# Kernel optimization log

Hardware: AMD Instinct MI355X
Metric: run time of the kernel (lower is better)

Reference implementation:

```python
import jax, jax.numpy as jnp
import numpy as np

N_EMBD = 1024
HEAD_SIZE = 64
B, T = 16, 2048


def setup_inputs() -> dict:
    key = jax.random.key(0)
    ks = jax.random.split(key, 7)
    s = 1.0 / np.sqrt(N_EMBD)
    return {
        "x": jax.random.normal(ks[0], (B, T, N_EMBD), dtype=jnp.float32),
        "Wq": jax.random.uniform(ks[1], (N_EMBD, HEAD_SIZE), jnp.float32, -s, s),
        "bq": jax.random.uniform(ks[2], (HEAD_SIZE,), jnp.float32, -s, s),
        "Wk": jax.random.uniform(ks[3], (N_EMBD, HEAD_SIZE), jnp.float32, -s, s),
        "bk": jax.random.uniform(ks[4], (HEAD_SIZE,), jnp.float32, -s, s),
        "Wv": jax.random.uniform(ks[5], (N_EMBD, HEAD_SIZE), jnp.float32, -s, s),
        "bv": jax.random.uniform(ks[6], (HEAD_SIZE,), jnp.float32, -s, s),
    }


def reference(x, Wq, bq, Wk, bk, Wv, bv):
    # x: [B, T, C]
    q = x @ Wq + bq          # [B, T, H]
    k = x @ Wk + bk          # [B, T, H]
    v = x @ Wv + bv          # [B, T, H]
    scale = k.shape[-1] ** -0.5
    wei = jnp.einsum("bth,bsh->bts", q, k) * scale  # [B, T, T]
    Tn = x.shape[1]
    causal = jnp.tril(jnp.ones((Tn, Tn), dtype=bool))
    wei = jnp.where(causal, wei, -jnp.inf)
    wei = jax.nn.softmax(wei, axis=-1)
    # dropout is identity in eval mode
    return jnp.einsum("bts,bsh->bth", wei, v)  # [B, T, H]
```

## Files before the change

kernel.cpp:

```cpp
#include <hip/hip_runtime.h>
#include <math.h>

#define BB 16
#define TT 2048
#define CC 1024
#define HH 64
#define MTOT (BB*TT)

typedef _Float16 f16;
typedef _Float16 f16x8 __attribute__((ext_vector_type(8)));
typedef float f32x4 __attribute__((ext_vector_type(4)));

#define WT_OFF 0
#define Q_OFF  196608
#define K_OFF  (Q_OFF + (size_t)MTOT*HH)
#define VT_OFF (K_OFF + (size_t)MTOT*HH)

__device__ __forceinline__ void async16(const void* g, void* l) {
    __builtin_amdgcn_global_load_lds(
        (const __attribute__((address_space(1))) unsigned int*)g,
        (__attribute__((address_space(3))) unsigned int*)l, 16, 0, 0);
}

__device__ __forceinline__ f16x8 cvt8(float4 u, float4 v) {
    f16x8 r;
    r[0] = (f16)u.x; r[1] = (f16)u.y; r[2] = (f16)u.z; r[3] = (f16)u.w;
    r[4] = (f16)v.x; r[5] = (f16)v.y; r[6] = (f16)v.z; r[7] = (f16)v.w;
    return r;
}

__global__ __launch_bounds__(256) void prep_kernel(
    const float* __restrict__ Wq, const float* __restrict__ Wk,
    const float* __restrict__ Wv, f16* __restrict__ ws)
{
    int e = blockIdx.x * 256 + threadIdx.x;
    int ng = e >> 10, k = e & 1023;
    int which = ng >> 6, n = ng & 63;
    const float* W = (which == 0) ? Wq : (which == 1) ? Wk : Wv;
    ws[WT_OFF + e] = (f16)W[k * HH + n];
}

__global__ __launch_bounds__(256, 2) void qkv_kernel(
    const float* __restrict__ x,
    const float* __restrict__ bq, const float* __restrict__ bk,
    const float* __restrict__ bv, f16* __restrict__ ws)
{
    __shared__ __align__(16) float Xs[64 * 64];
    __shared__ __align__(16) f16   Ws[192 * 64];
    __shared__ __align__(16) f16   Vt[64][72];

    const f16* wt = ws + WT_OFF;
    const int tid  = threadIdx.x;
    const int lane = tid & 63, w = tid >> 6;
    const int c = lane & 15, g = lane >> 4;
    const int m0 = blockIdx.x * 64;

    f32x4 acc[4][3];
    #pragma unroll
    for (int mt = 0; mt < 4; ++mt)
        #pragma unroll
        for (int j = 0; j < 3; ++j) acc[mt][j] = (f32x4){0.f, 0.f, 0.f, 0.f};

    for (int k0 = 0; k0 < CC; k0 += 64) {
        __syncthreads();
        #pragma unroll
        for (int i = 0; i < 4; ++i) {
            int G0 = (w * 4 + i) * 64;
            int G = G0 + lane;
            int r = G >> 4, q = G & 15;
            async16(x + (size_t)(m0 + r) * CC + k0 + ((q ^ (r & 15)) << 2),
                    Xs + G0 * 4);
        }
        #pragma unroll
        for (int i = 0; i < 6; ++i) {
            int G0 = (w * 6 + i) * 64;
            int G = G0 + lane;
            int r = G >> 3, q = G & 7;
            async16(wt + (size_t)r * CC + k0 + ((q ^ (r & 7)) << 3),
                    Ws + G0 * 8);
        }
        __syncthreads();

        #pragma unroll
        for (int kk = 0; kk < 2; ++kk) {
            f16x8 bfr[3];
            #pragma unroll
            for (int j = 0; j < 3; ++j) {
                int r = (3 * w + j) * 16 + c;
                int p = (kk * 4 + g) ^ (c & 7);
                bfr[j] = *(const f16x8*)(Ws + r * 64 + p * 8);
            }
            #pragma unroll
            for (int mt = 0; mt < 4; ++mt) {
                int r = mt * 16 + c;
                int q = kk * 8 + 2 * g;
                float4 f0 = *(const float4*)(Xs + r * 64 + (q ^ c) * 4);
                float4 f1 = *(const float4*)(Xs + r * 64 + ((q + 1) ^ c) * 4);
                f16x8 a = cvt8(f0, f1);
                #pragma unroll
                for (int j = 0; j < 3; ++j)
                    acc[mt][j] = __builtin_amdgcn_mfma_f32_16x16x32_f16(
                        a, bfr[j], acc[mt][j], 0, 0, 0);
            }
        }
    }

    #pragma unroll
    for (int j = 0; j < 3; ++j) {
        int nt = 3 * w + j;
        int plane = nt >> 2;
        int h = (nt & 3) * 16 + c;
        if (plane == 0) {
            float bias = bq[h];
            #pragma unroll
            for (int mt = 0; mt < 4; ++mt)
                #pragma unroll
                for (int r = 0; r < 4; ++r) {
                    int m = m0 + mt * 16 + 4 * g + r;
                    ws[Q_OFF + (size_t)m * HH + h] =
                        (f16)((acc[mt][j][r] + bias) * 0.125f);
                }
        } else if (plane == 1) {
            float bias = bk[h];
            #pragma unroll
            for (int mt = 0; mt < 4; ++mt)
                #pragma unroll
                for (int r = 0; r < 4; ++r) {
                    int m = m0 + mt * 16 + 4 * g + r;
                    ws[K_OFF + (size_t)m * HH + h] = (f16)(acc[mt][j][r] + bias);
                }
        } else {
            float bias = bv[h];
            #pragma unroll
            for (int mt = 0; mt < 4; ++mt)
                #pragma unroll
                for (int r = 0; r < 4; ++r)
                    Vt[h][mt * 16 + 4 * g + r] = (f16)(acc[mt][j][r] + bias);
        }
    }
    __syncthreads();
    {
        int h = tid >> 2, seg = tid & 3;
        f16* dst = ws + VT_OFF + (size_t)h * MTOT + m0 + seg * 16;
        *(f16x8*)dst       = *(f16x8*)&Vt[h][seg * 16];
        *(f16x8*)(dst + 8) = *(f16x8*)&Vt[h][seg * 16 + 8];
    }
}

__global__ __launch_bounds__(256, 2) void attn_kernel(
    const f16* __restrict__ ws, float* __restrict__ out)
{
    const f16* qp = ws + Q_OFF;
    const f16* kp = ws + K_OFF;
    const f16* vt = ws + VT_OFF;

    __shared__ __align__(16) f16 Qs[64 * 64];
    __shared__ __align__(16) f16 Ks[64 * 64];
    __shared__ __align__(16) f16 Vs[64 * 64];
    __shared__ __align__(16) f16 Ps[4][16][72];

    const int tid  = threadIdx.x;
    const int lane = tid & 63, w = tid >> 6;
    const int c = lane & 15, g = lane >> 4;

    const int id = blockIdx.x;
    const int r8 = id & 7, j = id >> 3;
    const int half = j >> 5, qr = j & 31;
    const int b  = 2 * r8 + half;
    const int qi = half ? (31 - qr) : qr;
    const int q0 = qi * 64;
    const size_t rowbase = (size_t)b * TT;

    #pragma unroll
    for (int i = 0; i < 2; ++i) {
        int G0 = (w * 2 + i) * 64;
        int G = G0 + lane;
        int r = G >> 3, q = G & 7;
        async16(qp + (rowbase + q0 + r) * HH + ((q ^ (r & 7)) << 3),
                Qs + G0 * 8);
    }

    f32x4 o[5];
    #pragma unroll
    for (int nt = 0; nt < 5; ++nt) o[nt] = (f32x4){0.f, 0.f, 0.f, 0.f};

    f16x8 onesf;
    #pragma unroll
    for (int i = 0; i < 8; ++i) onesf[i] = (c == 0) ? (f16)1.0f : (f16)0.0f;

    for (int st = 0; st <= qi; ++st) {
        const int s0 = st * 64;
        __syncthreads();
        #pragma unroll
        for (int i = 0; i < 2; ++i) {
            int G0 = (w * 2 + i) * 64;
            int G = G0 + lane;
            int r = G >> 3, q = G & 7;
            int sw = (q ^ (r & 7)) << 3;
            async16(kp + (rowbase + s0 + r) * HH + sw, Ks + G0 * 8);
            async16(vt + (size_t)r * MTOT + rowbase + s0 + sw, Vs + G0 * 8);
        }
        __syncthreads();

        f16x8 aq[2];
        {
            int r = w * 16 + c;
            aq[0] = *(const f16x8*)(Qs + r * 64 + ((g)     ^ (c & 7)) * 8);
            aq[1] = *(const f16x8*)(Qs + r * 64 + ((4 + g) ^ (c & 7)) * 8);
        }

        f32x4 s[4];
        #pragma unroll
        for (int nt = 0; nt < 4; ++nt) {
            s[nt] = (f32x4){0.f, 0.f, 0.f, 0.f};
            int r = nt * 16 + c;
            f16x8 b0 = *(const f16x8*)(Ks + r * 64 + ((g)     ^ (c & 7)) * 8);
            f16x8 b1 = *(const f16x8*)(Ks + r * 64 + ((4 + g) ^ (c & 7)) * 8);
            s[nt] = __builtin_amdgcn_mfma_f32_16x16x32_f16(aq[0], b0, s[nt], 0, 0, 0);
            s[nt] = __builtin_amdgcn_mfma_f32_16x16x32_f16(aq[1], b1, s[nt], 0, 0, 0);
        }

        if (st == qi) {
            #pragma unroll
            for (int nt = 0; nt < 4; ++nt)
                #pragma unroll
                for (int rr = 0; rr < 4; ++rr)
                    if (nt * 16 + c > w * 16 + 4 * g + rr) s[nt][rr] = -INFINITY;
        }

        #pragma unroll
        for (int nt = 0; nt < 4; ++nt)
            #pragma unroll
            for (int rr = 0; rr < 4; ++rr)
                Ps[w][4 * g + rr][nt * 16 + c] = (f16)__expf(s[nt][rr]);
        f16x8 pa0 = *(f16x8*)&Ps[w][c][g * 8];
        f16x8 pa1 = *(f16x8*)&Ps[w][c][32 + g * 8];

        #pragma unroll
        for (int nt = 0; nt < 4; ++nt) {
            int r = nt * 16 + c;
            f16x8 v0 = *(const f16x8*)(Vs + r * 64 + ((g)     ^ (c & 7)) * 8);
            f16x8 v1 = *(const f16x8*)(Vs + r * 64 + ((4 + g) ^ (c & 7)) * 8);
            o[nt] = __builtin_amdgcn_mfma_f32_16x16x32_f16(pa0, v0, o[nt], 0, 0, 0);
            o[nt] = __builtin_amdgcn_mfma_f32_16x16x32_f16(pa1, v1, o[nt], 0, 0, 0);
        }
        o[4] = __builtin_amdgcn_mfma_f32_16x16x32_f16(pa0, onesf, o[4], 0, 0, 0);
        o[4] = __builtin_amdgcn_mfma_f32_16x16x32_f16(pa1, onesf, o[4], 0, 0, 0);
    }

    #pragma unroll
    for (int rr = 0; rr < 4; ++rr) {
        float lv = __shfl(o[4][rr], lane & 48);
        float inv = 1.0f / lv;
        int mrow = q0 + w * 16 + 4 * g + rr;
        #pragma unroll
        for (int nt = 0; nt < 4; ++nt)
            out[(rowbase + mrow) * HH + nt * 16 + c] = o[nt][rr] * inv;
    }
}

extern "C" void kernel_launch(void* const* d_in, const int* in_sizes, int n_in,
                              void* d_out, int out_size, void* d_ws, size_t ws_size,
                              hipStream_t stream) {
    const float* x  = (const float*)d_in[0];
    const float* Wq = (const float*)d_in[1];
    const float* bq = (const float*)d_in[2];
    const float* Wk = (const float*)d_in[3];
    const float* bk = (const float*)d_in[4];
    const float* Wv = (const float*)d_in[5];
    const float* bv = (const float*)d_in[6];
    f16*   ws  = (f16*)d_ws;
    float* out = (float*)d_out;

    prep_kernel<<<768, 256, 0, stream>>>(Wq, Wk, Wv, ws);
    qkv_kernel<<<MTOT / 64, 256, 0, stream>>>(x, bq, bk, bv, ws);
    dim3 g2(512);
    attn_kernel<<<g2, 256, 0, stream>>>(ws, out);
}
```

Measured before the change: 242.9 us.

## Double-buffer K/V and X/W tiles with manual waitcnt; transpose weights via LDS

```diff
diff --git a/kernel.cpp b/kernel.cpp
--- a/kernel.cpp
+++ b/kernel.cpp
@@ -8,6 +8,7 @@
 #define MTOT (BB*TT)
 
 typedef _Float16 f16;
+typedef _Float16 f16x4 __attribute__((ext_vector_type(4)));
 typedef _Float16 f16x8 __attribute__((ext_vector_type(8)));
 typedef float f32x4 __attribute__((ext_vector_type(4)));
 
@@ -16,28 +17,48 @@
 #define K_OFF  (Q_OFF + (size_t)MTOT*HH)
 #define VT_OFF (K_OFF + (size_t)MTOT*HH)
 
+#define WAITV(n) asm volatile("s_waitcnt vmcnt(" #n ")" ::: "memory")
+#define WAITLGKM0 asm volatile("s_waitcnt lgkmcnt(0)" ::: "memory")
+
+__device__ __forceinline__ void bar_raw() {
+    asm volatile("" ::: "memory");
+    __builtin_amdgcn_s_barrier();
+    asm volatile("" ::: "memory");
+}
+
 __device__ __forceinline__ void async16(const void* g, void* l) {
     __builtin_amdgcn_global_load_lds(
         (const __attribute__((address_space(1))) unsigned int*)g,
         (__attribute__((address_space(3))) unsigned int*)l, 16, 0, 0);
 }
 
-__device__ __forceinline__ f16x8 cvt8(float4 u, float4 v) {
-    f16x8 r;
-    r[0] = (f16)u.x; r[1] = (f16)u.y; r[2] = (f16)u.z; r[3] = (f16)u.w;
-    r[4] = (f16)v.x; r[5] = (f16)v.y; r[6] = (f16)v.z; r[7] = (f16)v.w;
-    return r;
-}
-
 __global__ __launch_bounds__(256) void prep_kernel(
     const float* __restrict__ Wq, const float* __restrict__ Wk,
     const float* __restrict__ Wv, f16* __restrict__ ws)
 {
-    int e = blockIdx.x * 256 + threadIdx.x;
-    int ng = e >> 10, k = e & 1023;
-    int which = ng >> 6, n = ng & 63;
+    __shared__ f16 Ls[64][72];
+    const int which = blockIdx.x >> 4, k0 = (blockIdx.x & 15) * 64;
     const float* W = (which == 0) ? Wq : (which == 1) ? Wk : Wv;
-    ws[WT_OFF + e] = (f16)W[k * HH + n];
+    const int t = threadIdx.x;
+    const int kr = t >> 2, cb = t & 3;
+    #pragma unroll
+    for (int i = 0; i < 4; ++i) {
+        float4 v = *(const float4*)(W + (size_t)(k0 + kr) * HH + cb * 16 + i * 4);
+        Ls[kr][cb * 16 + i * 4 + 0] = (f16)v.x;
+        Ls[kr][cb * 16 + i * 4 + 1] = (f16)v.y;
+        Ls[kr][cb * 16 + i * 4 + 2] = (f16)v.z;
+        Ls[kr][cb * 16 + i * 4 + 3] = (f16)v.w;
+    }
+    __syncthreads();
+    const int n = t >> 2, kc = (t & 3) * 16;
+    f16x8 o0, o1;
+    #pragma unroll
+    for (int i = 0; i < 8; ++i) o0[i] = Ls[kc + i][n];
+    #pragma unroll
+    for (int i = 0; i < 8; ++i) o1[i] = Ls[kc + 8 + i][n];
+    f16* dst = ws + WT_OFF + (size_t)(which * 64 + n) * CC + k0 + kc;
+    *(f16x8*)dst = o0;
+    *(f16x8*)(dst + 8) = o1;
 }
 
 __global__ __launch_bounds__(256, 2) void qkv_kernel(
@@ -45,9 +66,9 @@
     const float* __restrict__ bq, const float* __restrict__ bk,
     const float* __restrict__ bv, f16* __restrict__ ws)
 {
-    __shared__ __align__(16) float Xs[64 * 64];
-    __shared__ __align__(16) f16   Ws[192 * 64];
-    __shared__ __align__(16) f16   Vt[64][72];
+    __shared__ __align__(16) f16 XsL[2][64 * 64];
+    __shared__ __align__(16) f16 WsL[2][192 * 64];
+    __shared__ __align__(16) f16 Vt[64][72];
 
     const f16* wt = ws + WT_OFF;
     const int tid  = threadIdx.x;
@@ -61,47 +82,70 @@
         #pragma unroll
         for (int j = 0; j < 3; ++j) acc[mt][j] = (f32x4){0.f, 0.f, 0.f, 0.f};
 
-    for (int k0 = 0; k0 < CC; k0 += 64) {
-        __syncthreads();
-        #pragma unroll
-        for (int i = 0; i < 4; ++i) {
-            int G0 = (w * 4 + i) * 64;
-            int G = G0 + lane;
-            int r = G >> 4, q = G & 15;
-            async16(x + (size_t)(m0 + r) * CC + k0 + ((q ^ (r & 15)) << 2),
-                    Xs + G0 * 4);
-        }
-        #pragma unroll
-        for (int i = 0; i < 6; ++i) {
-            int G0 = (w * 6 + i) * 64;
-            int G = G0 + lane;
-            int r = G >> 3, q = G & 7;
-            async16(wt + (size_t)r * CC + k0 + ((q ^ (r & 7)) << 3),
-                    Ws + G0 * 8);
-        }
-        __syncthreads();
-
+    float4 xr[4];
+
+    #pragma unroll
+    for (int i = 0; i < 4; ++i)
+        xr[i] = *(const float4*)(x + (size_t)(m0 + w * 16 + 4 * i + g) * CC + 4 * c);
+    #pragma unroll
+    for (int i = 0; i < 6; ++i) {
+        int G = (w * 6 + i) * 64 + lane;
+        int r = G >> 3, q = G & 7;
+        async16(wt + (size_t)r * CC + ((q ^ (r & 7)) << 3), &WsL[0][(w * 6 + i) * 512]);
+    }
+    #pragma unroll
+    for (int i = 0; i < 4; ++i) {
+        int r = w * 16 + 4 * i + g;
+        f16x4 h; h[0] = (f16)xr[i].x; h[1] = (f16)xr[i].y;
+                 h[2] = (f16)xr[i].z; h[3] = (f16)xr[i].w;
+        *(f16x4*)((char*)&XsL[0][0] + r * 128 + (((c >> 1) ^ (r & 7)) << 4) + (c & 1) * 8) = h;
+    }
+    __syncthreads();
+
+    for (int t = 0; t < 16; ++t) {
+        const int p = t & 1;
+        if (t < 15) {
+            const int k0 = (t + 1) * 64;
+            #pragma unroll
+            for (int i = 0; i < 4; ++i)
+                xr[i] = *(const float4*)(x + (size_t)(m0 + w * 16 + 4 * i + g) * CC + k0 + 4 * c);
+            #pragma unroll
+            for (int i = 0; i < 6; ++i) {
+                int G = (w * 6 + i) * 64 + lane;
+                int r = G >> 3, q = G & 7;
+                async16(wt + (size_t)r * CC + k0 + ((q ^ (r & 7)) << 3),
+                        &WsL[p ^ 1][(w * 6 + i) * 512]);
+            }
+        }
+        const f16* Xp = &XsL[p][0];
+        const f16* Wp = &WsL[p][0];
         #pragma unroll
         for (int kk = 0; kk < 2; ++kk) {
             f16x8 bfr[3];
             #pragma unroll
             for (int j = 0; j < 3; ++j) {
                 int r = (3 * w + j) * 16 + c;
-                int p = (kk * 4 + g) ^ (c & 7);
-                bfr[j] = *(const f16x8*)(Ws + r * 64 + p * 8);
+                bfr[j] = *(const f16x8*)(Wp + r * 64 + (((kk * 4 + g) ^ (c & 7)) << 3));
             }
             #pragma unroll
             for (int mt = 0; mt < 4; ++mt) {
                 int r = mt * 16 + c;
-                int q = kk * 8 + 2 * g;
-                float4 f0 = *(const float4*)(Xs + r * 64 + (q ^ c) * 4);
-                float4 f1 = *(const float4*)(Xs + r * 64 + ((q + 1) ^ c) * 4);
-                f16x8 a = cvt8(f0, f1);
+                f16x8 a = *(const f16x8*)(Xp + r * 64 + (((kk * 4 + g) ^ (c & 7)) << 3));
                 #pragma unroll
                 for (int j = 0; j < 3; ++j)
                     acc[mt][j] = __builtin_amdgcn_mfma_f32_16x16x32_f16(
                         a, bfr[j], acc[mt][j], 0, 0, 0);
             }
+        }
+        if (t < 15) {
+            #pragma unroll
+            for (int i = 0; i < 4; ++i) {
+                int r = w * 16 + 4 * i + g;
+                f16x4 h; h[0] = (f16)xr[i].x; h[1] = (f16)xr[i].y;
+                         h[2] = (f16)xr[i].z; h[3] = (f16)xr[i].w;
+                *(f16x4*)((char*)&XsL[p ^ 1][0] + r * 128 + (((c >> 1) ^ (r & 7)) << 4) + (c & 1) * 8) = h;
+            }
+            __syncthreads();
         }
     }
 
@@ -155,8 +199,8 @@
     const f16* vt = ws + VT_OFF;
 
     __shared__ __align__(16) f16 Qs[64 * 64];
-    __shared__ __align__(16) f16 Ks[64 * 64];
-    __shared__ __align__(16) f16 Vs[64 * 64];
+    __shared__ __align__(16) f16 KsL[2][64 * 64];
+    __shared__ __align__(16) f16 VsL[2][64 * 64];
     __shared__ __align__(16) f16 Ps[4][16][72];
 
     const int tid  = threadIdx.x;
@@ -173,51 +217,65 @@
 
     #pragma unroll
     for (int i = 0; i < 2; ++i) {
-        int G0 = (w * 2 + i) * 64;
-        int G = G0 + lane;
+        int G = (w * 2 + i) * 64 + lane;
         int r = G >> 3, q = G & 7;
-        async16(qp + (rowbase + q0 + r) * HH + ((q ^ (r & 7)) << 3),
-                Qs + G0 * 8);
-    }
-
-    f32x4 o[5];
-    #pragma unroll
-    for (int nt = 0; nt < 5; ++nt) o[nt] = (f32x4){0.f, 0.f, 0.f, 0.f};
-
-    f16x8 onesf;
-    #pragma unroll
-    for (int i = 0; i < 8; ++i) onesf[i] = (c == 0) ? (f16)1.0f : (f16)0.0f;
-
-    for (int st = 0; st <= qi; ++st) {
-        const int s0 = st * 64;
-        __syncthreads();
+        async16(qp + (rowbase + q0 + r) * HH + ((q ^ (r & 7)) << 3), Qs + (w * 2 + i) * 512);
+    }
+    #pragma unroll
+    for (int i = 0; i < 2; ++i) {
+        int G = (w * 2 + i) * 64 + lane;
+        int r = G >> 3, q = G & 7;
+        int sw = (q ^ (r & 7)) << 3;
+        async16(kp + (rowbase + r) * HH + sw, &KsL[0][(w * 2 + i) * 512]);
+        async16(vt + (size_t)r * MTOT + rowbase + sw, &VsL[0][(w * 2 + i) * 512]);
+    }
+    if (qi >= 1) {
         #pragma unroll
         for (int i = 0; i < 2; ++i) {
-            int G0 = (w * 2 + i) * 64;
-            int G = G0 + lane;
+            int G = (w * 2 + i) * 64 + lane;
             int r = G >> 3, q = G & 7;
             int sw = (q ^ (r & 7)) << 3;
-            async16(kp + (rowbase + s0 + r) * HH + sw, Ks + G0 * 8);
-            async16(vt + (size_t)r * MTOT + rowbase + s0 + sw, Vs + G0 * 8);
-        }
-        __syncthreads();
-
-        f16x8 aq[2];
-        {
-            int r = w * 16 + c;
-            aq[0] = *(const f16x8*)(Qs + r * 64 + ((g)     ^ (c & 7)) * 8);
-            aq[1] = *(const f16x8*)(Qs + r * 64 + ((4 + g) ^ (c & 7)) * 8);
-        }
+            async16(kp + (rowbase + 64 + r) * HH + sw, &KsL[1][(w * 2 + i) * 512]);
+            async16(vt + (size_t)r * MTOT + rowbase + 64 + sw, &VsL[1][(w * 2 + i) * 512]);
+        }
+        WAITV(8);
+    } else {
+        WAITV(4);
+    }
+
+    f16x8 aq0, aq1;
+    {
+        int r = w * 16 + c;
+        aq0 = *(const f16x8*)(Qs + r * 64 + ((g       ^ (c & 7)) << 3));
+        aq1 = *(const f16x8*)(Qs + r * 64 + (((4 + g) ^ (c & 7)) << 3));
+    }
+
+    f32x4 o[5];
+    #pragma unroll
+    for (int nt = 0; nt < 5; ++nt) o[nt] = (f32x4){0.f, 0.f, 0.f, 0.f};
+
+    f16x8 onesf;
+    #pragma unroll
+    for (int i = 0; i < 8; ++i) onesf[i] = (c == 0) ? (f16)1.0f : (f16)0.0f;
+
+    for (int st = 0; st <= qi; ++st) {
+        const int p = st & 1;
+        if (st < qi) { WAITV(4); }
+        else         { WAITV(0); }
+        bar_raw();
+
+        const f16* Kp = &KsL[p][0];
+        const f16* Vp = &VsL[p][0];
 
         f32x4 s[4];
         #pragma unroll
         for (int nt = 0; nt < 4; ++nt) {
             s[nt] = (f32x4){0.f, 0.f, 0.f, 0.f};
             int r = nt * 16 + c;
-            f16x8 b0 = *(const f16x8*)(Ks + r * 64 + ((g)     ^ (c & 7)) * 8);
-            f16x8 b1 = *(const f16x8*)(Ks + r * 64 + ((4 + g) ^ (c & 7)) * 8);
-            s[nt] = __builtin_amdgcn_mfma_f32_16x16x32_f16(aq[0], b0, s[nt], 0, 0, 0);
-            s[nt] = __builtin_amdgcn_mfma_f32_16x16x32_f16(aq[1], b1, s[nt], 0, 0, 0);
+            f16x8 b0 = *(const f16x8*)(Kp + r * 64 + ((g       ^ (c & 7)) << 3));
+            f16x8 b1 = *(const f16x8*)(Kp + r * 64 + (((4 + g) ^ (c & 7)) << 3));
+            s[nt] = __builtin_amdgcn_mfma_f32_16x16x32_f16(aq0, b0, s[nt], 0, 0, 0);
+            s[nt] = __builtin_amdgcn_mfma_f32_16x16x32_f16(aq1, b1, s[nt], 0, 0, 0);
         }
 
         if (st == qi) {
@@ -239,13 +297,27 @@
         #pragma unroll
         for (int nt = 0; nt < 4; ++nt) {
             int r = nt * 16 + c;
-            f16x8 v0 = *(const f16x8*)(Vs + r * 64 + ((g)     ^ (c & 7)) * 8);
-            f16x8 v1 = *(const f16x8*)(Vs + r * 64 + ((4 + g) ^ (c & 7)) * 8);
+            f16x8 v0 = *(const f16x8*)(Vp + r * 64 + ((g       ^ (c & 7)) << 3));
+            f16x8 v1 = *(const f16x8*)(Vp + r * 64 + (((4 + g) ^ (c & 7)) << 3));
             o[nt] = __builtin_amdgcn_mfma_f32_16x16x32_f16(pa0, v0, o[nt], 0, 0, 0);
             o[nt] = __builtin_amdgcn_mfma_f32_16x16x32_f16(pa1, v1, o[nt], 0, 0, 0);
         }
         o[4] = __builtin_amdgcn_mfma_f32_16x16x32_f16(pa0, onesf, o[4], 0, 0, 0);
         o[4] = __builtin_amdgcn_mfma_f32_16x16x32_f16(pa1, onesf, o[4], 0, 0, 0);
+
+        WAITLGKM0;
+        bar_raw();
+        if (st + 2 <= qi) {
+            const int s2 = (st + 2) * 64;
+            #pragma unroll
+            for (int i = 0; i < 2; ++i) {
+                int G = (w * 2 + i) * 64 + lane;
+                int r = G >> 3, q = G & 7;
+                int sw = (q ^ (r & 7)) << 3;
+                async16(kp + (rowbase + s2 + r) * HH + sw, &KsL[p][(w * 2 + i) * 512]);
+                async16(vt + (size_t)r * MTOT + rowbase + s2 + sw, &VsL[p][(w * 2 + i) * 512]);
+            }
+        }
     }
 
     #pragma unroll
@@ -272,8 +344,7 @@
     f16*   ws  = (f16*)d_ws;
     float* out = (float*)d_out;
 
-    prep_kernel<<<768, 256, 0, stream>>>(Wq, Wk, Wv, ws);
+    prep_kernel<<<48, 256, 0, stream>>>(Wq, Wk, Wv, ws);
     qkv_kernel<<<MTOT / 64, 256, 0, stream>>>(x, bq, bk, bv, ws);
-    dim3 g2(512);
-    attn_kernel<<<g2, 256, 0, stream>>>(ws, out);
-}
+    attn_kernel<<<512, 256, 0, stream>>>(ws, out);
+}
```

After: 251.9 us. 1.04x slower.

## Halve attention query tile to 32 rows, load Q to registers, use exp2 with prescaled Q

Applied to the files above, without the earlier changes.

```diff
diff --git a/kernel.cpp b/kernel.cpp
--- a/kernel.cpp
+++ b/kernel.cpp
@@ -33,11 +33,29 @@
     const float* __restrict__ Wq, const float* __restrict__ Wk,
     const float* __restrict__ Wv, f16* __restrict__ ws)
 {
-    int e = blockIdx.x * 256 + threadIdx.x;
-    int ng = e >> 10, k = e & 1023;
-    int which = ng >> 6, n = ng & 63;
+    __shared__ f16 Ls[64][72];
+    const int which = blockIdx.x >> 4, k0 = (blockIdx.x & 15) * 64;
     const float* W = (which == 0) ? Wq : (which == 1) ? Wk : Wv;
-    ws[WT_OFF + e] = (f16)W[k * HH + n];
+    const int t = threadIdx.x;
+    const int kr = t >> 2, cb = t & 3;
+    #pragma unroll
+    for (int i = 0; i < 4; ++i) {
+        float4 v = *(const float4*)(W + (size_t)(k0 + kr) * HH + cb * 16 + i * 4);
+        Ls[kr][cb * 16 + i * 4 + 0] = (f16)v.x;
+        Ls[kr][cb * 16 + i * 4 + 1] = (f16)v.y;
+        Ls[kr][cb * 16 + i * 4 + 2] = (f16)v.z;
+        Ls[kr][cb * 16 + i * 4 + 3] = (f16)v.w;
+    }
+    __syncthreads();
+    const int n = t >> 2, kc = (t & 3) * 16;
+    f16x8 o0, o1;
+    #pragma unroll
+    for (int i = 0; i < 8; ++i) o0[i] = Ls[kc + i][n];
+    #pragma unroll
+    for (int i = 0; i < 8; ++i) o1[i] = Ls[kc + 8 + i][n];
+    f16* dst = ws + WT_OFF + (size_t)(which * 64 + n) * CC + k0 + kc;
+    *(f16x8*)dst = o0;
+    *(f16x8*)(dst + 8) = o1;
 }
 
 __global__ __launch_bounds__(256, 2) void qkv_kernel(
@@ -105,6 +123,7 @@
         }
     }
 
+    const float QSCALE = 0.125f * 1.44269504089f;
     #pragma unroll
     for (int j = 0; j < 3; ++j) {
         int nt = 3 * w + j;
@@ -118,7 +137,7 @@
                 for (int r = 0; r < 4; ++r) {
                     int m = m0 + mt * 16 + 4 * g + r;
                     ws[Q_OFF + (size_t)m * HH + h] =
-                        (f16)((acc[mt][j][r] + bias) * 0.125f);
+                        (f16)((acc[mt][j][r] + bias) * QSCALE);
                 }
         } else if (plane == 1) {
             float bias = bk[h];
@@ -147,17 +166,16 @@
     }
 }
 
-__global__ __launch_bounds__(256, 2) void attn_kernel(
+__global__ __launch_bounds__(128, 3) void attn_kernel(
     const f16* __restrict__ ws, float* __restrict__ out)
 {
     const f16* qp = ws + Q_OFF;
     const f16* kp = ws + K_OFF;
     const f16* vt = ws + VT_OFF;
 
-    __shared__ __align__(16) f16 Qs[64 * 64];
     __shared__ __align__(16) f16 Ks[64 * 64];
     __shared__ __align__(16) f16 Vs[64 * 64];
-    __shared__ __align__(16) f16 Ps[4][16][72];
+    __shared__ __align__(16) f16 Ps[2][16][72];
 
     const int tid  = threadIdx.x;
     const int lane = tid & 63, w = tid >> 6;
@@ -165,20 +183,16 @@
 
     const int id = blockIdx.x;
     const int r8 = id & 7, j = id >> 3;
-    const int half = j >> 5, qr = j & 31;
+    const int half = j >> 6, qr = j & 63;
     const int b  = 2 * r8 + half;
-    const int qi = half ? (31 - qr) : qr;
-    const int q0 = qi * 64;
+    const int qi = half ? (63 - qr) : qr;
+    const int q0 = qi * 32;
+    const int stmax = qi >> 1;
     const size_t rowbase = (size_t)b * TT;
 
-    #pragma unroll
-    for (int i = 0; i < 2; ++i) {
-        int G0 = (w * 2 + i) * 64;
-        int G = G0 + lane;
-        int r = G >> 3, q = G & 7;
-        async16(qp + (rowbase + q0 + r) * HH + ((q ^ (r & 7)) << 3),
-                Qs + G0 * 8);
-    }
+    const f16* qrow = qp + (rowbase + q0 + w * 16 + c) * HH;
+    const f16x8 aq0 = *(const f16x8*)(qrow + 8 * g);
+    const f16x8 aq1 = *(const f16x8*)(qrow + 32 + 8 * g);
 
     f32x4 o[5];
     #pragma unroll
@@ -188,12 +202,12 @@
     #pragma unroll
     for (int i = 0; i < 8; ++i) onesf[i] = (c == 0) ? (f16)1.0f : (f16)0.0f;
 
-    for (int st = 0; st <= qi; ++st) {
+    for (int st = 0; st <= stmax; ++st) {
         const int s0 = st * 64;
         __syncthreads();
         #pragma unroll
-        for (int i = 0; i < 2; ++i) {
-            int G0 = (w * 2 + i) * 64;
+        for (int i = 0; i < 4; ++i) {
+            int G0 = (w * 4 + i) * 64;
             int G = G0 + lane;
             int r = G >> 3, q = G & 7;
             int sw = (q ^ (r & 7)) << 3;
@@ -202,45 +216,40 @@
         }
         __syncthreads();
 
-        f16x8 aq[2];
-        {
-            int r = w * 16 + c;
-            aq[0] = *(const f16x8*)(Qs + r * 64 + ((g)     ^ (c & 7)) * 8);
-            aq[1] = *(const f16x8*)(Qs + r * 64 + ((4 + g) ^ (c & 7)) * 8);
-        }
-
         f32x4 s[4];
         #pragma unroll
         for (int nt = 0; nt < 4; ++nt) {
             s[nt] = (f32x4){0.f, 0.f, 0.f, 0.f};
             int r = nt * 16 + c;
-            f16x8 b0 = *(const f16x8*)(Ks + r * 64 + ((g)     ^ (c & 7)) * 8);
-            f16x8 b1 = *(const f16x8*)(Ks + r * 64 + ((4 + g) ^ (c & 7)) * 8);
-            s[nt] = __builtin_amdgcn_mfma_f32_16x16x32_f16(aq[0], b0, s[nt], 0, 0, 0);
-            s[nt] = __builtin_amdgcn_mfma_f32_16x16x32_f16(aq[1], b1, s[nt], 0, 0, 0);
-        }
-
-        if (st == qi) {
+            f16x8 b0 = *(const f16x8*)(Ks + r * 64 + ((g       ^ (c & 7)) << 3));
+            f16x8 b1 = *(const f16x8*)(Ks + r * 64 + (((4 + g) ^ (c & 7)) << 3));
+            s[nt] = __builtin_amdgcn_mfma_f32_16x16x32_f16(aq0, b0, s[nt], 0, 0, 0);
+            s[nt] = __builtin_amdgcn_mfma_f32_16x16x32_f16(aq1, b1, s[nt], 0, 0, 0);
+        }
+
+        if (st == stmax) {
+            const int doff = q0 - s0;
             #pragma unroll
             for (int nt = 0; nt < 4; ++nt)
                 #pragma unroll
                 for (int rr = 0; rr < 4; ++rr)
-                    if (nt * 16 + c > w * 16 + 4 * g + rr) s[nt][rr] = -INFINITY;
+                    if (nt * 16 + c > doff + w * 16 + 4 * g + rr)
+                        s[nt][rr] = -INFINITY;
         }
 
         #pragma unroll
         for (int nt = 0; nt < 4; ++nt)
             #pragma unroll
             for (int rr = 0; rr < 4; ++rr)
-                Ps[w][4 * g + rr][nt * 16 + c] = (f16)__expf(s[nt][rr]);
+                Ps[w][4 * g + rr][nt * 16 + c] = (f16)__builtin_exp2f(s[nt][rr]);
         f16x8 pa0 = *(f16x8*)&Ps[w][c][g * 8];
         f16x8 pa1 = *(f16x8*)&Ps[w][c][32 + g * 8];
 
         #pragma unroll
         for (int nt = 0; nt < 4; ++nt) {
             int r = nt * 16 + c;
-            f16x8 v0 = *(const f16x8*)(Vs + r * 64 + ((g)     ^ (c & 7)) * 8);
-            f16x8 v1 = *(const f16x8*)(Vs + r * 64 + ((4 + g) ^ (c & 7)) * 8);
+            f16x8 v0 = *(const f16x8*)(Vs + r * 64 + ((g       ^ (c & 7)) << 3));
+            f16x8 v1 = *(const f16x8*)(Vs + r * 64 + (((4 + g) ^ (c & 7)) << 3));
             o[nt] = __builtin_amdgcn_mfma_f32_16x16x32_f16(pa0, v0, o[nt], 0, 0, 0);
             o[nt] = __builtin_amdgcn_mfma_f32_16x16x32_f16(pa1, v1, o[nt], 0, 0, 0);
         }
@@ -272,8 +281,7 @@
     f16*   ws  = (f16*)d_ws;
     float* out = (float*)d_out;
 
-    prep_kernel<<<768, 256, 0, stream>>>(Wq, Wk, Wv, ws);
+    prep_kernel<<<48, 256, 0, stream>>>(Wq, Wk, Wv, ws);
     qkv_kernel<<<MTOT / 64, 256, 0, stream>>>(x, bq, bk, bv, ws);
-    dim3 g2(512);
-    attn_kernel<<<g2, 256, 0, stream>>>(ws, out);
-}
+    attn_kernel<<<1024, 128, 0, stream>>>(ws, out);
+}
```

After: 248.3 us. +2.2%, slower.
